# Performance work log

Hardware: AMD Instinct MI355X
Metric: run time of the kernel (lower is better)

The kernel has to match this reference:

```python
import jax, jax.numpy as jnp
import numpy as np

B = 8192
N_IN = 1024
N_OUT = 1024
IN_OUT = N_IN + N_OUT


def setup_inputs() -> dict:
    key = jax.random.key(0)
    ks = jax.random.split(key, 11)
    s = 1.0 / np.sqrt(IN_OUT)  # nn.Linear default init scale
    inp = {
        "x": jax.random.normal(ks[0], (B, N_IN), dtype=jnp.float32),
        "out_tm1": jax.random.normal(ks[1], (B, N_OUT), dtype=jnp.float32),
        "state_tm1": jax.random.normal(ks[2], (B, N_OUT), dtype=jnp.float32),
        "Wf": jax.random.uniform(ks[3], (IN_OUT, N_OUT), jnp.float32, -s, s),
        "bf": jax.random.uniform(ks[4], (N_OUT,), jnp.float32, -s, s),
        "Wi": jax.random.uniform(ks[5], (IN_OUT, N_OUT), jnp.float32, -s, s),
        "bi": jax.random.uniform(ks[6], (N_OUT,), jnp.float32, -s, s),
        "Wc": jax.random.uniform(ks[7], (IN_OUT, N_OUT), jnp.float32, -s, s),
        "bc": jax.random.uniform(ks[8], (N_OUT,), jnp.float32, -s, s),
        "Wo": jax.random.uniform(ks[9], (IN_OUT, N_OUT), jnp.float32, -s, s),
        "bo": jax.random.uniform(ks[10], (N_OUT,), jnp.float32, -s, s),
    }
    return inp


def reference(x, out_tm1, state_tm1, Wf, bf, Wi, bi, Wc, bc, Wo, bo):
    xh = jnp.concatenate((x, out_tm1), axis=-1)  # [B, n_in+n_out]
    f = jax.nn.sigmoid(xh @ Wf + bf)             # forget gate
    i = jax.nn.sigmoid(xh @ Wi + bi)             # input gate
    c = jnp.tanh(xh @ Wc + bc)                   # candidates
    o = jax.nn.sigmoid(xh @ Wo + bo)             # output gate
    new_state = state_tm1 * f + i * c
    output_t = o * jnp.tanh(new_state)
    return (output_t, new_state)
```

## Files before the change

### kernel.cpp

```cpp
#include <hip/hip_runtime.h>

#define B_DIM 8192
#define NOUT  1024
#define KDIM  2048
#define NCI   4096

typedef __bf16 bf16x8 __attribute__((ext_vector_type(8)));
typedef float  f32x4  __attribute__((ext_vector_type(4)));

__device__ __forceinline__ unsigned short f2bf(float f) {
  unsigned int u = __float_as_uint(f);
  u += 0x7fff + ((u >> 16) & 1);
  return (unsigned short)(u >> 16);
}
__device__ __forceinline__ float sigmoid_f(float x) {
  return 1.0f / (1.0f + __expf(-x));
}
__device__ __forceinline__ float tanh_f(float x) {
  return 1.0f - 2.0f / (__expf(2.0f * x) + 1.0f);
}
__device__ __forceinline__ void gload_lds16(const void* g, void* l) {
  __builtin_amdgcn_global_load_lds(
      (const __attribute__((address_space(1))) void*)g,
      (__attribute__((address_space(3))) void*)l, 16, 0, 0);
}

__device__ __forceinline__ int cimap(int g, int n) {
  return ((n >> 6) << 8) | ((g >> 1) << 7) | (((n >> 4) & 3) << 5) |
         ((g & 1) << 4) | (n & 15);
}

__global__ void pack_xh_kernel(const float* __restrict__ x,
                               const float* __restrict__ h,
                               unsigned short* __restrict__ xh) {
  const long total = (long)B_DIM * KDIM / 4;
  for (long i = (long)blockIdx.x * blockDim.x + threadIdx.x; i < total;
       i += (long)gridDim.x * blockDim.x) {
    long e = i * 4;
    int b = (int)(e >> 11);
    int c = (int)(e & 2047);
    float4 v = (c < 1024)
        ? *reinterpret_cast<const float4*>(x + (long)b * 1024 + c)
        : *reinterpret_cast<const float4*>(h + (long)b * 1024 + (c - 1024));
    ushort4 o;
    o.x = f2bf(v.x); o.y = f2bf(v.y); o.z = f2bf(v.z); o.w = f2bf(v.w);
    *reinterpret_cast<ushort4*>(xh + e) = o;
  }
}

__global__ void transpose_w_kernel(const float* __restrict__ Wf,
                                   const float* __restrict__ Wi,
                                   const float* __restrict__ Wc,
                                   const float* __restrict__ Wo,
                                   unsigned short* __restrict__ wt) {
  __shared__ float tile[32][33];
  const int g = blockIdx.z;
  const float* W = (g == 0) ? Wf : (g == 1) ? Wi : (g == 2) ? Wc : Wo;
  const int n0 = blockIdx.x * 32;
  const int k0 = blockIdx.y * 32;
  const int tx = threadIdx.x, ty = threadIdx.y;
#pragma unroll
  for (int r = ty; r < 32; r += 8)
    tile[r][tx] = W[(long)(k0 + r) * NOUT + n0 + tx];
  __syncthreads();
#pragma unroll
  for (int r = ty; r < 32; r += 8) {
    int ci = cimap(g, n0 + r);
    wt[(long)ci * KDIM + k0 + tx] = f2bf(tile[tx][r]);
  }
}

#define BAR()   { __builtin_amdgcn_s_barrier(); __builtin_amdgcn_sched_barrier(0); }
#define LGKM0() asm volatile("s_waitcnt lgkmcnt(0)" ::: "memory")
#define VM4()   asm volatile("s_waitcnt vmcnt(4)" ::: "memory")
#define VM0()   asm volatile("s_waitcnt vmcnt(0)" ::: "memory")

__device__ __forceinline__ void stage_half(const char* g, long grow0, int kt,
                                           char* ldsm, int base,
                                           int wave, int lane) {
  const int rsub = lane >> 3;
  const int scol = (((lane & 7) ^ rsub) << 4);
  const long rowb = (grow0 + wave * 8 + rsub) * 4096 + (long)kt * 128 + scol;
  gload_lds16(g + rowb,               ldsm + base + wave * 1024);
  gload_lds16(g + rowb + 64L * 4096,  ldsm + base + 8192 + wave * 1024);
}

#define LOAD_A(BUF, MQ)                                                     \
  _Pragma("unroll") for (int mi = 0; mi < 4; ++mi) {                        \
    const char* p_ = lds + (BUF)*32768 + (MQ)*16384 +                       \
                     (wm * 64 + mi * 16 + lrow) * 128;                      \
    af[mi][0] = *reinterpret_cast<const bf16x8*>(p_ + colA0);               \
    af[mi][1] = *reinterpret_cast<const bf16x8*>(p_ + colA1);               \
  }

#define LOAD_B(BUF, NQ)                                                     \
  _Pragma("unroll") for (int ni = 0; ni < 2; ++ni) {                        \
    const char* p_ = lds + 65536 + (BUF)*32768 + (NQ)*16384 +               \
                     (wn * 32 + ni * 16 + lrow) * 128;                      \
    bq[ni][0] = *reinterpret_cast<const bf16x8*>(p_ + colA0);               \
    bq[ni][1] = *reinterpret_cast<const bf16x8*>(p_ + colA1);               \
  }

#define MFMA16(MQ, NQ)                                                     \
  __builtin_amdgcn_s_setprio(1);                                            \
  _Pragma("unroll") for (int mi = 0; mi < 4; ++mi)                          \
  _Pragma("unroll") for (int ni = 0; ni < 2; ++ni)                          \
  _Pragma("unroll") for (int s = 0; s < 2; ++s)                             \
    acc[MQ][NQ][mi][ni] = __builtin_amdgcn_mfma_f32_16x16x32_bf16(          \
        af[mi][s], bq[ni][s], acc[MQ][NQ][mi][ni], 0, 0, 0);                \
  __builtin_amdgcn_s_setprio(0);

__global__ __launch_bounds__(512, 2)
void lstm_gemm_kernel(const unsigned short* __restrict__ xh,
                      const unsigned short* __restrict__ wt,
                      const float* __restrict__ state,
                      const float* __restrict__ bfp,
                      const float* __restrict__ bip,
                      const float* __restrict__ bcp,
                      const float* __restrict__ bop,
                      float* __restrict__ out) {
  __shared__ __attribute__((aligned(128))) char lds[131072];

  const int tid  = threadIdx.x;
  const int wave = tid >> 6;
  const int lane = tid & 63;
  const int wm = wave >> 2;
  const int wn = wave & 3;

  int wg = blockIdx.y * 16 + blockIdx.x;
  wg = (wg & 7) * 64 + (wg >> 3);
  const int  bm = wg >> 4;
  const int  bn = wg & 15;
  const long m0 = (long)bm * 256;
  const long n0 = (long)bn * 256;

  const int lrow  = lane & 15;
  const int csw   = (lane & 7) << 4;
  const int ck    = (lane >> 4) << 4;
  const int colA0 = ck ^ csw;
  const int colA1 = (64 | ck) ^ csw;

  const char* xh_b = (const char*)xh;
  const char* wt_b = (const char*)wt;

  stage_half(xh_b, m0,        0, lds, 0,             wave, lane);
  stage_half(xh_b, m0 + 128,  0, lds, 16384,         wave, lane);
  stage_half(wt_b, n0,        0, lds, 65536,         wave, lane);
  stage_half(wt_b, n0 + 128,  0, lds, 65536 + 16384, wave, lane);
  stage_half(xh_b, m0,        1, lds, 32768,         wave, lane);
  stage_half(wt_b, n0 + 128,  1, lds, 65536 + 32768 + 16384, wave, lane);

  f32x4 acc[2][2][4][2] = {};
  bf16x8 af[4][2];
  bf16x8 bq[2][2];

  VM4();
  BAR();

  for (int t = 0; t < 32; t += 2) {
    const int k1 = (t + 1 <= 31) ? t + 1 : 31;
    const int k2 = (t + 2 <= 31) ? t + 2 : 31;
    const int k3 = (t + 3 <= 31) ? t + 3 : 31;

    LOAD_A(0, 0) LOAD_B(0, 0)
    stage_half(xh_b, m0 + 128, k1, lds, 32768 + 16384, wave, lane);
    BAR(); LGKM0(); MFMA16(0, 0) BAR();
    LOAD_B(0, 1)
    stage_half(wt_b, n0, k1, lds, 65536 + 32768, wave, lane);
    BAR(); LGKM0(); MFMA16(0, 1) BAR();
    LOAD_A(0, 1)
    stage_half(xh_b, m0, k2, lds, 0, wave, lane);
    BAR(); LGKM0(); MFMA16(1, 1) BAR();
    LOAD_B(0, 0)
    stage_half(wt_b, n0 + 128, k2, lds, 65536 + 16384, wave, lane);
    BAR(); LGKM0(); MFMA16(1, 0) VM4(); BAR();

    LOAD_A(1, 0) LOAD_B(1, 0)
    stage_half(xh_b, m0 + 128, k2, lds, 16384, wave, lane);
    BAR(); LGKM0(); MFMA16(0, 0) BAR();
    LOAD_B(1, 1)
    stage_half(wt_b, n0, k2, lds, 65536, wave, lane);
    BAR(); LGKM0(); MFMA16(0, 1) BAR();
    LOAD_A(1, 1)
    stage_half(xh_b, m0, k3, lds, 32768, wave, lane);
    BAR(); LGKM0(); MFMA16(1, 1) BAR();
    LOAD_B(1, 0)
    stage_half(wt_b, n0 + 128, k3, lds, 65536 + 32768 + 16384, wave, lane);
    BAR(); LGKM0(); MFMA16(1, 0) VM4(); BAR();
  }
  VM0();

  const int   nout = bn * 64 + wn * 16 + lrow;
  const int   rsub4 = (lane >> 4) << 2;
  const float bfv = bfp[nout], biv = bip[nout];
  const float bcv = bcp[nout], bov = bop[nout];
  float* out2 = out + (long)B_DIM * NOUT;
#pragma unroll
  for (int mq = 0; mq < 2; ++mq)
#pragma unroll
    for (int mi = 0; mi < 4; ++mi)
#pragma unroll
      for (int v = 0; v < 4; ++v) {
        const long row = m0 + mq * 128 + wm * 64 + mi * 16 + rsub4 + v;
        float fg = sigmoid_f(acc[mq][0][mi][0][v] + bfv);
        float ig = sigmoid_f(acc[mq][0][mi][1][v] + biv);
        float cg = tanh_f   (acc[mq][1][mi][0][v] + bcv);
        float og = sigmoid_f(acc[mq][1][mi][1][v] + bov);
        float st = state[row * NOUT + nout];
        float ns = st * fg + ig * cg;
        out [row * NOUT + nout] = og * tanh_f(ns);
        out2[row * NOUT + nout] = ns;
      }
}

extern "C" void kernel_launch(void* const* d_in, const int* in_sizes, int n_in,
                              void* d_out, int out_size, void* d_ws, size_t ws_size,
                              hipStream_t stream) {
  const float* x     = (const float*)d_in[0];
  const float* h     = (const float*)d_in[1];
  const float* state = (const float*)d_in[2];
  const float* Wf    = (const float*)d_in[3];
  const float* bfp   = (const float*)d_in[4];
  const float* Wi    = (const float*)d_in[5];
  const float* bip   = (const float*)d_in[6];
  const float* Wc    = (const float*)d_in[7];
  const float* bcp   = (const float*)d_in[8];
  const float* Wo    = (const float*)d_in[9];
  const float* bop   = (const float*)d_in[10];
  float* out = (float*)d_out;

  unsigned short* xh = (unsigned short*)d_ws;
  unsigned short* wt = (unsigned short*)((char*)d_ws + (size_t)B_DIM * KDIM * 2);

  hipLaunchKernelGGL(pack_xh_kernel, dim3(2048), dim3(256), 0, stream, x, h, xh);
  hipLaunchKernelGGL(transpose_w_kernel, dim3(NOUT / 32, KDIM / 32, 4),
                     dim3(32, 8), 0, stream, Wf, Wi, Wc, Wo, wt);
  hipLaunchKernelGGL(lstm_gemm_kernel, dim3(16, 32), dim3(512), 0, stream,
                     xh, wt, state, bfp, bip, bcp, bop, out);
}
```

Baseline: 158.1 us.

## Restructure GEMM main loop with dual B fragment registers and one barrier per stage

Reworks the software pipeline of the bf16 MFMA GEMM main loop. B fragments now live in two register sets (bq0/bq1), so one quadrant's B can be reused without reloading from LDS, which drops one LDS read phase per half-iteration. Each stage now has a single barrier with a vmcnt(6) wait instead of two barriers plus an lgkmcnt(0) wait, and the global-to-LDS staging order is permuted to match. LDS addressing is hoisted into precomputed base pointers. This raises register pressure and depends on the new wait counts being correct for data hazards.

```diff
diff --git a/kernel.cpp b/kernel.cpp
--- a/kernel.cpp
+++ b/kernel.cpp
@@ -3,7 +3,6 @@
 #define B_DIM 8192
 #define NOUT  1024
 #define KDIM  2048
-#define NCI   4096
 
 typedef __bf16 bf16x8 __attribute__((ext_vector_type(8)));
 typedef float  f32x4  __attribute__((ext_vector_type(4)));
@@ -71,9 +70,9 @@
 }
 
 #define BAR()   { __builtin_amdgcn_s_barrier(); __builtin_amdgcn_sched_barrier(0); }
-#define LGKM0() asm volatile("s_waitcnt lgkmcnt(0)" ::: "memory")
-#define VM4()   asm volatile("s_waitcnt vmcnt(4)" ::: "memory")
-#define VM0()   asm volatile("s_waitcnt vmcnt(0)" ::: "memory")
+#define VM6()   { asm volatile("s_waitcnt vmcnt(6)" ::: "memory"); }
+#define VM4()   { asm volatile("s_waitcnt vmcnt(4)" ::: "memory"); }
+#define VM0()   { asm volatile("s_waitcnt vmcnt(0)" ::: "memory"); }
 
 __device__ __forceinline__ void stage_half(const char* g, long grow0, int kt,
                                            char* ldsm, int base,
@@ -85,29 +84,29 @@
   gload_lds16(g + rowb + 64L * 4096,  ldsm + base + 8192 + wave * 1024);
 }
 
-#define LOAD_A(BUF, MQ)                                                     \
+#define LOAD_AF(BUF, MQ)                                                    \
   _Pragma("unroll") for (int mi = 0; mi < 4; ++mi) {                        \
-    const char* p_ = lds + (BUF)*32768 + (MQ)*16384 +                       \
-                     (wm * 64 + mi * 16 + lrow) * 128;                      \
-    af[mi][0] = *reinterpret_cast<const bf16x8*>(p_ + colA0);               \
-    af[mi][1] = *reinterpret_cast<const bf16x8*>(p_ + colA1);               \
-  }
-
-#define LOAD_B(BUF, NQ)                                                     \
+    af[mi][0] = *reinterpret_cast<const bf16x8*>(                           \
+        baseA0 + (BUF)*32768 + (MQ)*16384 + mi*2048);                       \
+    af[mi][1] = *reinterpret_cast<const bf16x8*>(                           \
+        baseA1 + (BUF)*32768 + (MQ)*16384 + mi*2048);                       \
+  }
+
+#define LOAD_BQ(BUF, NQ, DST)                                               \
   _Pragma("unroll") for (int ni = 0; ni < 2; ++ni) {                        \
-    const char* p_ = lds + 65536 + (BUF)*32768 + (NQ)*16384 +               \
-                     (wn * 32 + ni * 16 + lrow) * 128;                      \
-    bq[ni][0] = *reinterpret_cast<const bf16x8*>(p_ + colA0);               \
-    bq[ni][1] = *reinterpret_cast<const bf16x8*>(p_ + colA1);               \
-  }
-
-#define MFMA16(MQ, NQ)                                                     \
+    DST[ni][0] = *reinterpret_cast<const bf16x8*>(                          \
+        baseB0 + (BUF)*32768 + (NQ)*16384 + ni*2048);                       \
+    DST[ni][1] = *reinterpret_cast<const bf16x8*>(                          \
+        baseB1 + (BUF)*32768 + (NQ)*16384 + ni*2048);                       \
+  }
+
+#define MFMA16(MQ, NQ, BQ)                                                  \
   __builtin_amdgcn_s_setprio(1);                                            \
   _Pragma("unroll") for (int mi = 0; mi < 4; ++mi)                          \
   _Pragma("unroll") for (int ni = 0; ni < 2; ++ni)                          \
   _Pragma("unroll") for (int s = 0; s < 2; ++s)                             \
     acc[MQ][NQ][mi][ni] = __builtin_amdgcn_mfma_f32_16x16x32_bf16(          \
-        af[mi][s], bq[ni][s], acc[MQ][NQ][mi][ni], 0, 0, 0);                \
+        af[mi][s], BQ[ni][s], acc[MQ][NQ][mi][ni], 0, 0, 0);                \
   __builtin_amdgcn_s_setprio(0);
 
 __global__ __launch_bounds__(512, 2)
@@ -140,53 +139,64 @@
   const int colA0 = ck ^ csw;
   const int colA1 = (64 | ck) ^ csw;
 
+  const char* baseA0 = lds + (wm * 64 + lrow) * 128 + colA0;
+  const char* baseA1 = lds + (wm * 64 + lrow) * 128 + colA1;
+  const char* baseB0 = lds + 65536 + (wn * 32 + lrow) * 128 + colA0;
+  const char* baseB1 = lds + 65536 + (wn * 32 + lrow) * 128 + colA1;
+
   const char* xh_b = (const char*)xh;
   const char* wt_b = (const char*)wt;
 
-  stage_half(xh_b, m0,        0, lds, 0,             wave, lane);
-  stage_half(xh_b, m0 + 128,  0, lds, 16384,         wave, lane);
-  stage_half(wt_b, n0,        0, lds, 65536,         wave, lane);
-  stage_half(wt_b, n0 + 128,  0, lds, 65536 + 16384, wave, lane);
-  stage_half(xh_b, m0,        1, lds, 32768,         wave, lane);
-  stage_half(wt_b, n0 + 128,  1, lds, 65536 + 32768 + 16384, wave, lane);
+  stage_half(xh_b, m0,        0, lds, 0,                     wave, lane);
+  stage_half(wt_b, n0,        0, lds, 65536,                 wave, lane);
+  stage_half(wt_b, n0 + 128,  0, lds, 65536 + 16384,         wave, lane);
+  stage_half(xh_b, m0 + 128,  0, lds, 16384,                 wave, lane);
+  stage_half(xh_b, m0,        1, lds, 32768,                 wave, lane);
+  stage_half(wt_b, n0,        1, lds, 65536 + 32768,         wave, lane);
 
   f32x4 acc[2][2][4][2] = {};
   bf16x8 af[4][2];
-  bf16x8 bq[2][2];
+  bf16x8 bq0[2][2];
+  bf16x8 bq1[2][2];
 
   VM4();
   BAR();
 
   for (int t = 0; t < 32; t += 2) {
-    const int k1 = (t + 1 <= 31) ? t + 1 : 31;
-    const int k2 = (t + 2 <= 31) ? t + 2 : 31;
-    const int k3 = (t + 3 <= 31) ? t + 3 : 31;
-
-    LOAD_A(0, 0) LOAD_B(0, 0)
-    stage_half(xh_b, m0 + 128, k1, lds, 32768 + 16384, wave, lane);
-    BAR(); LGKM0(); MFMA16(0, 0) BAR();
-    LOAD_B(0, 1)
-    stage_half(wt_b, n0, k1, lds, 65536 + 32768, wave, lane);
-    BAR(); LGKM0(); MFMA16(0, 1) BAR();
-    LOAD_A(0, 1)
-    stage_half(xh_b, m0, k2, lds, 0, wave, lane);
-    BAR(); LGKM0(); MFMA16(1, 1) BAR();
-    LOAD_B(0, 0)
-    stage_half(wt_b, n0 + 128, k2, lds, 65536 + 16384, wave, lane);
-    BAR(); LGKM0(); MFMA16(1, 0) VM4(); BAR();
-
-    LOAD_A(1, 0) LOAD_B(1, 0)
-    stage_half(xh_b, m0 + 128, k2, lds, 16384, wave, lane);
-    BAR(); LGKM0(); MFMA16(0, 0) BAR();
-    LOAD_B(1, 1)
-    stage_half(wt_b, n0, k2, lds, 65536, wave, lane);
-    BAR(); LGKM0(); MFMA16(0, 1) BAR();
-    LOAD_A(1, 1)
-    stage_half(xh_b, m0, k3, lds, 32768, wave, lane);
-    BAR(); LGKM0(); MFMA16(1, 1) BAR();
-    LOAD_B(1, 0)
-    stage_half(wt_b, n0 + 128, k3, lds, 65536 + 32768 + 16384, wave, lane);
-    BAR(); LGKM0(); MFMA16(1, 0) VM4(); BAR();
+    const int k2c = (t + 2 > 31) ? 31 : t + 2;
+    const int k3c = (t + 3 > 31) ? 31 : t + 3;
+
+    LOAD_AF(0, 0) LOAD_BQ(0, 0, bq0)
+    stage_half(wt_b, n0 + 128, t + 1, lds, 65536 + 32768 + 16384, wave, lane);
+    VM6(); BAR();
+    MFMA16(0, 0, bq0)
+    LOAD_BQ(0, 1, bq1)
+    stage_half(xh_b, m0 + 128, t + 1, lds, 32768 + 16384, wave, lane);
+    VM6(); BAR();
+    MFMA16(0, 1, bq1)
+    LOAD_AF(0, 1)
+    stage_half(xh_b, m0, k2c, lds, 0, wave, lane);
+    VM6(); BAR();
+    MFMA16(1, 1, bq1)
+    stage_half(wt_b, n0, k2c, lds, 65536, wave, lane);
+    VM6(); BAR();
+    MFMA16(1, 0, bq0)
+
+    LOAD_AF(1, 0) LOAD_BQ(1, 0, bq0)
+    stage_half(wt_b, n0 + 128, k2c, lds, 65536 + 16384, wave, lane);
+    VM6(); BAR();
+    MFMA16(0, 0, bq0)
+    LOAD_BQ(1, 1, bq1)
+    stage_half(xh_b, m0 + 128, k2c, lds, 16384, wave, lane);
+    VM6(); BAR();
+    MFMA16(0, 1, bq1)
+    LOAD_AF(1, 1)
+    stage_half(xh_b, m0, k3c, lds, 32768, wave, lane);
+    VM6(); BAR();
+    MFMA16(1, 1, bq1)
+    stage_half(wt_b, n0, k3c, lds, 65536 + 32768, wave, lane);
+    VM6(); BAR();
+    MFMA16(1, 0, bq0)
   }
   VM0();
 
```

New measurement: 153.3 us. 1.03x faster.

## Retile LSTM GEMM to 128x256 blocks with triple-buffered 32-wide K pipeline

Applied to the files above, without the earlier changes.

Replaces the 256x256 tile, 512-thread, double-buffered 64-wide-K GEMM with a 128x256 tile on 256 threads. Each wave now owns a full 128-row strip and 4 gates by 16 outputs, and the K loop uses 32-wide slices in a three-stage LDS ring with one barrier per step. The weight interleave mapping and the XCD-aware block remap are rewritten to match. The goal is fewer barriers and less LDS (72KB, so two blocks fit per CU) in exchange for lower operand reuse per block and more K iterations.

```diff
diff --git a/kernel.cpp b/kernel.cpp
--- a/kernel.cpp
+++ b/kernel.cpp
@@ -3,7 +3,6 @@
 #define B_DIM 8192
 #define NOUT  1024
 #define KDIM  2048
-#define NCI   4096
 
 typedef __bf16 bf16x8 __attribute__((ext_vector_type(8)));
 typedef float  f32x4  __attribute__((ext_vector_type(4)));
@@ -26,8 +25,7 @@
 }
 
 __device__ __forceinline__ int cimap(int g, int n) {
-  return ((n >> 6) << 8) | ((g >> 1) << 7) | (((n >> 4) & 3) << 5) |
-         ((g & 1) << 4) | (n & 15);
+  return ((n >> 4) << 6) | ((g & 3) << 4) | (n & 15);
 }
 
 __global__ void pack_xh_kernel(const float* __restrict__ x,
@@ -70,47 +68,47 @@
   }
 }
 
-#define BAR()   { __builtin_amdgcn_s_barrier(); __builtin_amdgcn_sched_barrier(0); }
-#define LGKM0() asm volatile("s_waitcnt lgkmcnt(0)" ::: "memory")
-#define VM4()   asm volatile("s_waitcnt vmcnt(4)" ::: "memory")
-#define VM0()   asm volatile("s_waitcnt vmcnt(0)" ::: "memory")
-
-__device__ __forceinline__ void stage_half(const char* g, long grow0, int kt,
-                                           char* ldsm, int base,
-                                           int wave, int lane) {
-  const int rsub = lane >> 3;
-  const int scol = (((lane & 7) ^ rsub) << 4);
-  const long rowb = (grow0 + wave * 8 + rsub) * 4096 + (long)kt * 128 + scol;
-  gload_lds16(g + rowb,               ldsm + base + wave * 1024);
-  gload_lds16(g + rowb + 64L * 4096,  ldsm + base + 8192 + wave * 1024);
-}
-
-#define LOAD_A(BUF, MQ)                                                     \
-  _Pragma("unroll") for (int mi = 0; mi < 4; ++mi) {                        \
-    const char* p_ = lds + (BUF)*32768 + (MQ)*16384 +                       \
-                     (wm * 64 + mi * 16 + lrow) * 128;                      \
-    af[mi][0] = *reinterpret_cast<const bf16x8*>(p_ + colA0);               \
-    af[mi][1] = *reinterpret_cast<const bf16x8*>(p_ + colA1);               \
-  }
-
-#define LOAD_B(BUF, NQ)                                                     \
-  _Pragma("unroll") for (int ni = 0; ni < 2; ++ni) {                        \
-    const char* p_ = lds + 65536 + (BUF)*32768 + (NQ)*16384 +               \
-                     (wn * 32 + ni * 16 + lrow) * 128;                      \
-    bq[ni][0] = *reinterpret_cast<const bf16x8*>(p_ + colA0);               \
-    bq[ni][1] = *reinterpret_cast<const bf16x8*>(p_ + colA1);               \
-  }
-
-#define MFMA16(MQ, NQ)                                                     \
+__device__ __forceinline__ void stage6(const char* xh_b, const char* wt_b,
+                                       long aoff, long boff, int kt,
+                                       char* lds, int sbase, int tid) {
+  const long kb = (long)kt * 64;
+#pragma unroll
+  for (int r = 0; r < 2; ++r)
+    gload_lds16(xh_b + aoff + (long)r * 64 * 4096 + kb,
+                lds + sbase + r * 4096 + tid * 16);
+#pragma unroll
+  for (int r = 0; r < 4; ++r)
+    gload_lds16(wt_b + boff + (long)r * 64 * 4096 + kb,
+                lds + sbase + 8192 + r * 4096 + tid * 16);
+}
+
+#define LOAD_FRAGS(S)                                                       \
+  _Pragma("unroll") for (int mi = 0; mi < 8; ++mi)                          \
+    af[mi] = *reinterpret_cast<const bf16x8*>(                              \
+        lds + (S)*24576 + mi * 1024 + rdoff);                               \
+  _Pragma("unroll") for (int ni = 0; ni < 4; ++ni)                          \
+    bq[ni] = *reinterpret_cast<const bf16x8*>(                              \
+        lds + (S)*24576 + 8192 + wn * 4096 + ni * 1024 + rdoff);
+
+#define MFMA32()                                                            \
+  _Pragma("unroll") for (int mi = 0; mi < 8; ++mi)                          \
+  _Pragma("unroll") for (int ni = 0; ni < 4; ++ni)                          \
+    acc[mi][ni] = __builtin_amdgcn_mfma_f32_16x16x32_bf16(                  \
+        af[mi], bq[ni], acc[mi][ni], 0, 0, 0);
+
+#define ITER(RS, WS, KST)                                                   \
+  LOAD_FRAGS(RS)                                                            \
+  stage6(xh_b, wt_b, aoff, boff, (KST), lds, (WS)*24576, tid);              \
+  asm volatile("s_waitcnt vmcnt(6) lgkmcnt(0)" ::: "memory");               \
+  __builtin_amdgcn_sched_barrier(0);                                        \
+  __builtin_amdgcn_s_barrier();                                             \
+  __builtin_amdgcn_sched_barrier(0);                                        \
   __builtin_amdgcn_s_setprio(1);                                            \
-  _Pragma("unroll") for (int mi = 0; mi < 4; ++mi)                          \
-  _Pragma("unroll") for (int ni = 0; ni < 2; ++ni)                          \
-  _Pragma("unroll") for (int s = 0; s < 2; ++s)                             \
-    acc[MQ][NQ][mi][ni] = __builtin_amdgcn_mfma_f32_16x16x32_bf16(          \
-        af[mi][s], bq[ni][s], acc[MQ][NQ][mi][ni], 0, 0, 0);                \
-  __builtin_amdgcn_s_setprio(0);
-
-__global__ __launch_bounds__(512, 2)
+  MFMA32()                                                                  \
+  __builtin_amdgcn_s_setprio(0);                                            \
+  __builtin_amdgcn_sched_barrier(0);
+
+__global__ __launch_bounds__(256, 2)
 void lstm_gemm_kernel(const unsigned short* __restrict__ xh,
                       const unsigned short* __restrict__ wt,
                       const float* __restrict__ state,
@@ -119,98 +117,76 @@
                       const float* __restrict__ bcp,
                       const float* __restrict__ bop,
                       float* __restrict__ out) {
-  __shared__ __attribute__((aligned(128))) char lds[131072];
+  __shared__ __attribute__((aligned(128))) char lds[73728];
 
   const int tid  = threadIdx.x;
-  const int wave = tid >> 6;
   const int lane = tid & 63;
-  const int wm = wave >> 2;
-  const int wn = wave & 3;
-
-  int wg = blockIdx.y * 16 + blockIdx.x;
-  wg = (wg & 7) * 64 + (wg >> 3);
-  const int  bm = wg >> 4;
-  const int  bn = wg & 15;
-  const long m0 = (long)bm * 256;
-  const long n0 = (long)bn * 256;
-
-  const int lrow  = lane & 15;
-  const int csw   = (lane & 7) << 4;
-  const int ck    = (lane >> 4) << 4;
-  const int colA0 = ck ^ csw;
-  const int colA1 = (64 | ck) ^ csw;
+  const int wn   = tid >> 6;
+
+  const int wgid = blockIdx.y * 16 + blockIdx.x;
+  const int j    = wgid >> 3;
+  const int xcd  = wgid & 7;
+  const int bx   = (xcd << 1) | (j & 1);
+  const int by   = j >> 1;
+  const long m0  = (long)by * 128;
+  const long c0  = (long)bx * 256;
+
+  const int  rsub = tid >> 2;
+  const int  gsw  = ((tid & 3) ^ (rsub & 3)) << 4;
+  const long aoff = (m0 + rsub) * 4096 + gsw;
+  const long boff = (c0 + rsub) * 4096 + gsw;
+
+  const int rdoff = (lane & 15) * 64 + (((lane >> 4) ^ (lane & 3)) << 4);
 
   const char* xh_b = (const char*)xh;
   const char* wt_b = (const char*)wt;
 
-  stage_half(xh_b, m0,        0, lds, 0,             wave, lane);
-  stage_half(xh_b, m0 + 128,  0, lds, 16384,         wave, lane);
-  stage_half(wt_b, n0,        0, lds, 65536,         wave, lane);
-  stage_half(wt_b, n0 + 128,  0, lds, 65536 + 16384, wave, lane);
-  stage_half(xh_b, m0,        1, lds, 32768,         wave, lane);
-  stage_half(wt_b, n0 + 128,  1, lds, 65536 + 32768 + 16384, wave, lane);
-
-  f32x4 acc[2][2][4][2] = {};
-  bf16x8 af[4][2];
-  bf16x8 bq[2][2];
-
-  VM4();
-  BAR();
-
-  for (int t = 0; t < 32; t += 2) {
-    const int k1 = (t + 1 <= 31) ? t + 1 : 31;
-    const int k2 = (t + 2 <= 31) ? t + 2 : 31;
-    const int k3 = (t + 3 <= 31) ? t + 3 : 31;
-
-    LOAD_A(0, 0) LOAD_B(0, 0)
-    stage_half(xh_b, m0 + 128, k1, lds, 32768 + 16384, wave, lane);
-    BAR(); LGKM0(); MFMA16(0, 0) BAR();
-    LOAD_B(0, 1)
-    stage_half(wt_b, n0, k1, lds, 65536 + 32768, wave, lane);
-    BAR(); LGKM0(); MFMA16(0, 1) BAR();
-    LOAD_A(0, 1)
-    stage_half(xh_b, m0, k2, lds, 0, wave, lane);
-    BAR(); LGKM0(); MFMA16(1, 1) BAR();
-    LOAD_B(0, 0)
-    stage_half(wt_b, n0 + 128, k2, lds, 65536 + 16384, wave, lane);
-    BAR(); LGKM0(); MFMA16(1, 0) VM4(); BAR();
-
-    LOAD_A(1, 0) LOAD_B(1, 0)
-    stage_half(xh_b, m0 + 128, k2, lds, 16384, wave, lane);
-    BAR(); LGKM0(); MFMA16(0, 0) BAR();
-    LOAD_B(1, 1)
-    stage_half(wt_b, n0, k2, lds, 65536, wave, lane);
-    BAR(); LGKM0(); MFMA16(0, 1) BAR();
-    LOAD_A(1, 1)
-    stage_half(xh_b, m0, k3, lds, 32768, wave, lane);
-    BAR(); LGKM0(); MFMA16(1, 1) BAR();
-    LOAD_B(1, 0)
-    stage_half(wt_b, n0 + 128, k3, lds, 65536 + 32768 + 16384, wave, lane);
-    BAR(); LGKM0(); MFMA16(1, 0) VM4(); BAR();
+  f32x4  acc[8][4] = {};
+  bf16x8 af[8];
+  bf16x8 bq[4];
+
+  stage6(xh_b, wt_b, aoff, boff, 0, lds, 0,     tid);
+  stage6(xh_b, wt_b, aoff, boff, 1, lds, 24576, tid);
+  asm volatile("s_waitcnt vmcnt(6)" ::: "memory");
+  __builtin_amdgcn_sched_barrier(0);
+  __builtin_amdgcn_s_barrier();
+  __builtin_amdgcn_sched_barrier(0);
+
+  for (int t = 0; t < 63; t += 3) {
+    const int k2 = t + 2;
+    const int k3 = (t + 3 > 63) ? 63 : t + 3;
+    const int k4 = (t + 4 > 63) ? 63 : t + 4;
+    ITER(0, 2, k2)
+    ITER(1, 0, k3)
+    ITER(2, 1, k4)
   }
-  VM0();
-
-  const int   nout = bn * 64 + wn * 16 + lrow;
+  LOAD_FRAGS(0)
+  asm volatile("s_waitcnt lgkmcnt(0)" ::: "memory");
+  __builtin_amdgcn_sched_barrier(0);
+  __builtin_amdgcn_s_setprio(1);
+  MFMA32()
+  __builtin_amdgcn_s_setprio(0);
+  asm volatile("s_waitcnt vmcnt(0)" ::: "memory");
+
+  const int   nout = (bx * 4 + wn) * 16 + (lane & 15);
   const int   rsub4 = (lane >> 4) << 2;
   const float bfv = bfp[nout], biv = bip[nout];
   const float bcv = bcp[nout], bov = bop[nout];
   float* out2 = out + (long)B_DIM * NOUT;
 #pragma unroll
-  for (int mq = 0; mq < 2; ++mq)
-#pragma unroll
-    for (int mi = 0; mi < 4; ++mi)
-#pragma unroll
-      for (int v = 0; v < 4; ++v) {
-        const long row = m0 + mq * 128 + wm * 64 + mi * 16 + rsub4 + v;
-        float fg = sigmoid_f(acc[mq][0][mi][0][v] + bfv);
-        float ig = sigmoid_f(acc[mq][0][mi][1][v] + biv);
-        float cg = tanh_f   (acc[mq][1][mi][0][v] + bcv);
-        float og = sigmoid_f(acc[mq][1][mi][1][v] + bov);
-        float st = state[row * NOUT + nout];
-        float ns = st * fg + ig * cg;
-        out [row * NOUT + nout] = og * tanh_f(ns);
-        out2[row * NOUT + nout] = ns;
-      }
+  for (int mi = 0; mi < 8; ++mi)
+#pragma unroll
+    for (int v = 0; v < 4; ++v) {
+      const long row = m0 + mi * 16 + rsub4 + v;
+      float fg = sigmoid_f(acc[mi][0][v] + bfv);
+      float ig = sigmoid_f(acc[mi][1][v] + biv);
+      float cg = tanh_f   (acc[mi][2][v] + bcv);
+      float og = sigmoid_f(acc[mi][3][v] + bov);
+      float st = state[row * NOUT + nout];
+      float ns = st * fg + ig * cg;
+      out [row * NOUT + nout] = og * tanh_f(ns);
+      out2[row * NOUT + nout] = ns;
+    }
 }
 
 extern "C" void kernel_launch(void* const* d_in, const int* in_sizes, int n_in,
@@ -235,6 +211,6 @@
   hipLaunchKernelGGL(pack_xh_kernel, dim3(2048), dim3(256), 0, stream, x, h, xh);
   hipLaunchKernelGGL(transpose_w_kernel, dim3(NOUT / 32, KDIM / 32, 4),
                      dim3(32, 8), 0, stream, Wf, Wi, Wc, Wo, wt);
-  hipLaunchKernelGGL(lstm_gemm_kernel, dim3(16, 32), dim3(512), 0, stream,
+  hipLaunchKernelGGL(lstm_gemm_kernel, dim3(16, 64), dim3(256), 0, stream,
                      xh, wt, state, bfp, bip, bcp, bop, out);
 }
```

New measurement: 173.0 us. 1.09x slower.
